# Optimization experiments

Measured on AMD Instinct MI355X. Metric: run time of the kernel, lower is better.

Reference implementation:

```python
import jax, jax.numpy as jnp
import numpy as np

N = 100000          # nodes
MUL = 64            # multiplicity of each irrep in input_1 (64x0e + 64x1o)
O0, O1M, O2M = 320, 128, 64   # output multiplicities: 320x0e + 128x1o + 64x1e
SQRT3 = float(np.sqrt(3.0))
SQRT6 = float(np.sqrt(6.0))
# e3nn path weights: sqrt(dim(ir_out) / sum_paths_to_out(mul1*mul2))
PW0 = float(1.0 / np.sqrt(2.0 * MUL))     # 0e: two paths, x = 128
PW1 = float(np.sqrt(3.0 / (2.0 * MUL)))   # 1o: two paths, x = 128
PW2 = float(np.sqrt(3.0 / MUL))           # 1e: one path,  x = 64


def setup_inputs() -> dict:
    key = jax.random.key(0)
    k = jax.random.split(key, 8)
    return {
        "input_1": jax.random.normal(k[0], (N, 4 * MUL), jnp.float32),  # 64x0e + 64x1o
        "input_2": jax.random.normal(k[1], (N, 4), jnp.float32),        # 1x0e + 1x1o
        "W_a0_o0": jax.random.normal(k[2], (MUL, O0), jnp.float32),     # 0e x 0e -> 0e
        "W_b1_o0": jax.random.normal(k[3], (MUL, O0), jnp.float32),     # 1o x 1o -> 0e
        "W_a1_o1": jax.random.normal(k[4], (MUL, O1M), jnp.float32),    # 0e x 1o -> 1o
        "W_b0_o1": jax.random.normal(k[5], (MUL, O1M), jnp.float32),    # 1o x 0e -> 1o
        "W_b1_o2": jax.random.normal(k[6], (MUL, O2M), jnp.float32),    # 1o x 1o -> 1e
        "bias": jnp.zeros((O0,), jnp.float32),                          # on the 0e scalars
    }


def reference(input_1, input_2, W_a0_o0, W_b1_o0, W_a1_o1, W_b0_o1, W_b1_o2, bias):
    n = input_1.shape[0]
    s_a = input_1[:, :MUL]                        # [N, MUL]      0e block
    v_b = input_1[:, MUL:].reshape(n, MUL, 3)     # [N, MUL, 3]   1o block
    s0 = input_2[:, :1]                           # [N, 1]        0e attr
    v1 = input_2[:, 1:]                           # [N, 3]        1o attr

    # --- 0e output: (0e*0e) and (1o.1o)/sqrt3 (CG delta_ij/sqrt3), fully-connected weights
    dot_b1 = jnp.einsum('nuk,nk->nu', v_b, v1)    # [N, MUL]
    o0 = PW0 * ((s_a * s0) @ W_a0_o0 + (dot_b1 / SQRT3) @ W_b1_o0) + bias  # [N, O0]

    # --- 1o output: (0e x 1o) and (1o x 0e), CG delta/sqrt3
    o1 = (PW1 / SQRT3) * (
        jnp.einsum('nu,uw->nw', s_a, W_a1_o1)[:, :, None] * v1[:, None, :]
        + jnp.einsum('nuk,uw->nwk', v_b, W_b0_o1) * s0[:, :, None]
    )                                             # [N, O1M, 3]

    # --- 1e output: (1o x 1o), CG eps_ijk/sqrt6 -> cross product
    cr = jnp.cross(v_b, v1[:, None, :])           # [N, MUL, 3]
    o2 = (PW2 / SQRT6) * jnp.einsum('nuk,uw->nwk', cr, W_b1_o2)  # [N, O2M, 3]

    return jnp.concatenate([o0, o1.reshape(n, -1), o2.reshape(n, -1)], axis=-1)  # [N, 896]
```

## Files before the change

### kernel.cpp

```cpp
#include <hip/hip_runtime.h>


typedef __bf16 v8bf __attribute__((ext_vector_type(8)));
typedef __bf16 v4bf __attribute__((ext_vector_type(4)));
typedef float f32x4 __attribute__((ext_vector_type(4)));

#define PW0f   0.08838834764831845f
#define PW0S3f 0.05103103630798288f


__global__ __launch_bounds__(256) void prep_weights(
    const float* __restrict__ Wa0, const float* __restrict__ Wb1o0,
    const float* __restrict__ Wa1, const float* __restrict__ Wb0,
    const float* __restrict__ Wo2, unsigned short* __restrict__ ws) {
  int t = blockIdx.x * 256 + threadIdx.x;
  float v; int k, n, base;
  if (t < 20480) {
    k = t / 320; n = t % 320; base = 0;     v = Wa0[k * 320 + n] * PW0f;
  } else if (t < 40960) {
    int tt = t - 20480; k = tt / 320; n = tt % 320; base = 20480; v = Wb1o0[k * 320 + n] * PW0S3f;
  } else if (t < 49152) {
    int tt = t - 40960; k = tt / 128; n = tt % 128; base = 40960; v = Wa1[k * 128 + n] * PW0f;
  } else if (t < 57344) {
    int tt = t - 49152; k = tt / 128; n = tt % 128; base = 49152; v = Wb0[k * 128 + n] * PW0f;
  } else {
    int tt = t - 57344; k = tt / 64;  n = tt % 64;  base = 57344; v = Wo2[k * 64 + n] * PW0f;
  }
  int nt = n >> 4, cc = n & 15, ks = k >> 5, qq = (k >> 3) & 3, j = k & 7;
  int addr = base + ((nt * 2 + ks) * 64 + qq * 16 + cc) * 8 + j;
  __bf16 h = (__bf16)v;
  ws[addr] = __builtin_bit_cast(unsigned short, h);
}

__global__ __launch_bounds__(256, 4) void tp_main(
    const float* __restrict__ in1, const float* __restrict__ in2,
    const float* __restrict__ bias, const unsigned short* __restrict__ wsb,
    float* __restrict__ out, int N) {
  __shared__ __attribute__((aligned(16))) float s0v1[16 * 4];
  __shared__ __attribute__((aligned(16))) __bf16 fsa[1024];
  __shared__ __attribute__((aligned(16))) __bf16 fvb[3][1024];

  const int tid = threadIdx.x;
  const int r0 = blockIdx.x * 16;

  {
    const int m = tid & 15;
    const int g = tid >> 4;
    int rr = r0 + m; if (rr >= N) rr = N - 1;
    const float* rp = in1 + (size_t)rr * 256;
    const float4 sa4 = *(const float4*)(rp + 4 * g);
    const float4 w0  = *(const float4*)(rp + 64 + 12 * g);
    const float4 w1  = *(const float4*)(rp + 64 + 12 * g + 4);
    const float4 w2  = *(const float4*)(rp + 64 + 12 * g + 8);
    const float vf[12] = {w0.x, w0.y, w0.z, w0.w, w1.x, w1.y, w1.z, w1.w,
                          w2.x, w2.y, w2.z, w2.w};
    const int wbase = (((g >> 3) * 64 + ((g >> 1) & 3) * 16 + m) * 8) + 4 * (g & 1);
    v4bf pk;
    pk[0] = (__bf16)sa4.x; pk[1] = (__bf16)sa4.y; pk[2] = (__bf16)sa4.z; pk[3] = (__bf16)sa4.w;
    *(v4bf*)(fsa + wbase) = pk;
#pragma unroll
    for (int c3 = 0; c3 < 3; ++c3) {
      pk[0] = (__bf16)vf[c3]; pk[1] = (__bf16)vf[3 + c3];
      pk[2] = (__bf16)vf[6 + c3]; pk[3] = (__bf16)vf[9 + c3];
      *(v4bf*)(fvb[c3] + wbase) = pk;
    }
    if (tid < 16) {
      int rr2 = r0 + tid; if (rr2 >= N) rr2 = N - 1;
      *(float4*)(s0v1 + tid * 4) = *(const float4*)(in2 + (size_t)rr2 * 4);
    }
  }
  __syncthreads();

  const int lane = tid & 63;
  const int wv = tid >> 6;
  const int c = lane & 15, q = lane >> 4;

  v8bf a_sa[2], a_vb[3][2];
#pragma unroll
  for (int ks = 0; ks < 2; ++ks) {
    a_sa[ks] = *(const v8bf*)(fsa + (ks * 64 + lane) * 8);
#pragma unroll
    for (int c3 = 0; c3 < 3; ++c3)
      a_vb[c3][ks] = *(const v8bf*)(fvb[c3] + (ks * 64 + lane) * 8);
  }
  float4 sv[4];
#pragma unroll
  for (int r = 0; r < 4; ++r) sv[r] = *(const float4*)(s0v1 + (q * 4 + r) * 4);

  const unsigned short* Wa0p = wsb;
  const unsigned short* Wb1p = wsb + 20480;
  const unsigned short* Wa1p = wsb + 40960;
  const unsigned short* Wb0p = wsb + 49152;
  const unsigned short* Wo2p = wsb + 57344;

  for (int job = wv; job < 32; job += 4) {
    if (job < 20) {
      const int nt = job;
      v8bf wa0 = *(const v8bf*)(Wa0p + ((nt * 2 + 0) * 64 + lane) * 8);
      v8bf wa1 = *(const v8bf*)(Wa0p + ((nt * 2 + 1) * 64 + lane) * 8);
      v8bf wb0 = *(const v8bf*)(Wb1p + ((nt * 2 + 0) * 64 + lane) * 8);
      v8bf wb1 = *(const v8bf*)(Wb1p + ((nt * 2 + 1) * 64 + lane) * 8);
      f32x4 ta = {0.f, 0.f, 0.f, 0.f};
      f32x4 tb[3]; tb[0] = ta; tb[1] = ta; tb[2] = ta;
      ta = __builtin_amdgcn_mfma_f32_16x16x32_bf16(a_sa[0], wa0, ta, 0, 0, 0);
      ta = __builtin_amdgcn_mfma_f32_16x16x32_bf16(a_sa[1], wa1, ta, 0, 0, 0);
#pragma unroll
      for (int c3 = 0; c3 < 3; ++c3) {
        tb[c3] = __builtin_amdgcn_mfma_f32_16x16x32_bf16(a_vb[c3][0], wb0, tb[c3], 0, 0, 0);
        tb[c3] = __builtin_amdgcn_mfma_f32_16x16x32_bf16(a_vb[c3][1], wb1, tb[c3], 0, 0, 0);
      }
      const int col = nt * 16 + c;
      const float bv = bias[col];
#pragma unroll
      for (int r = 0; r < 4; ++r) {
        const int gr = r0 + q * 4 + r;
        if (gr < N)
          out[(size_t)gr * 896 + col] =
              bv + sv[r].x * ta[r] + sv[r].y * tb[0][r] + sv[r].z * tb[1][r] + sv[r].w * tb[2][r];
      }
    } else if (job < 28) {
      const int jt = job - 20;
      v8bf ba0 = *(const v8bf*)(Wa1p + ((jt * 2 + 0) * 64 + lane) * 8);
      v8bf ba1 = *(const v8bf*)(Wa1p + ((jt * 2 + 1) * 64 + lane) * 8);
      v8bf bb0 = *(const v8bf*)(Wb0p + ((jt * 2 + 0) * 64 + lane) * 8);
      v8bf bb1 = *(const v8bf*)(Wb0p + ((jt * 2 + 1) * 64 + lane) * 8);
      f32x4 t1 = {0.f, 0.f, 0.f, 0.f};
      f32x4 t2[3]; t2[0] = t1; t2[1] = t1; t2[2] = t1;
      t1 = __builtin_amdgcn_mfma_f32_16x16x32_bf16(a_sa[0], ba0, t1, 0, 0, 0);
      t1 = __builtin_amdgcn_mfma_f32_16x16x32_bf16(a_sa[1], ba1, t1, 0, 0, 0);
#pragma unroll
      for (int c3 = 0; c3 < 3; ++c3) {
        t2[c3] = __builtin_amdgcn_mfma_f32_16x16x32_bf16(a_vb[c3][0], bb0, t2[c3], 0, 0, 0);
        t2[c3] = __builtin_amdgcn_mfma_f32_16x16x32_bf16(a_vb[c3][1], bb1, t2[c3], 0, 0, 0);
      }
#pragma unroll
      for (int r = 0; r < 4; ++r) {
        const int gr = r0 + q * 4 + r;
        if (gr < N) {
          const size_t base = (size_t)gr * 896 + 320 + 3 * (jt * 16 + c);
          out[base + 0] = t1[r] * sv[r].y + t2[0][r] * sv[r].x;
          out[base + 1] = t1[r] * sv[r].z + t2[1][r] * sv[r].x;
          out[base + 2] = t1[r] * sv[r].w + t2[2][r] * sv[r].x;
        }
      }
    } else {
      const int jt = job - 28;
      v8bf b0v = *(const v8bf*)(Wo2p + ((jt * 2 + 0) * 64 + lane) * 8);
      v8bf b1v = *(const v8bf*)(Wo2p + ((jt * 2 + 1) * 64 + lane) * 8);
      f32x4 t3[3];
      t3[0] = f32x4{0.f, 0.f, 0.f, 0.f}; t3[1] = t3[0]; t3[2] = t3[0];
#pragma unroll
      for (int c3 = 0; c3 < 3; ++c3) {
        t3[c3] = __builtin_amdgcn_mfma_f32_16x16x32_bf16(a_vb[c3][0], b0v, t3[c3], 0, 0, 0);
        t3[c3] = __builtin_amdgcn_mfma_f32_16x16x32_bf16(a_vb[c3][1], b1v, t3[c3], 0, 0, 0);
      }
#pragma unroll
      for (int r = 0; r < 4; ++r) {
        const int gr = r0 + q * 4 + r;
        if (gr < N) {
          const size_t base = (size_t)gr * 896 + 704 + 3 * (jt * 16 + c);
          out[base + 0] = t3[1][r] * sv[r].w - t3[2][r] * sv[r].z;
          out[base + 1] = t3[2][r] * sv[r].y - t3[0][r] * sv[r].w;
          out[base + 2] = t3[0][r] * sv[r].z - t3[1][r] * sv[r].y;
        }
      }
    }
  }
}

extern "C" void kernel_launch(void* const* d_in, const int* in_sizes, int n_in,
                              void* d_out, int out_size, void* d_ws, size_t ws_size,
                              hipStream_t stream) {
  const float* in1   = (const float*)d_in[0];
  const float* in2   = (const float*)d_in[1];
  const float* Wa0   = (const float*)d_in[2];
  const float* Wb1o0 = (const float*)d_in[3];
  const float* Wa1   = (const float*)d_in[4];
  const float* Wb0   = (const float*)d_in[5];
  const float* Wo2   = (const float*)d_in[6];
  const float* bias  = (const float*)d_in[7];
  float* out = (float*)d_out;
  unsigned short* ws = (unsigned short*)d_ws;

  const int N = in_sizes[0] / 256;

  hipLaunchKernelGGL(prep_weights, dim3(240), dim3(256), 0, stream,
                     Wa0, Wb1o0, Wa1, Wb0, Wo2, ws);
  const int nblocks = (N + 15) / 16;
  hipLaunchKernelGGL(tp_main, dim3(nblocks), dim3(256), 0, stream,
                     in1, in2, bias, ws, out, N);
}
```

Before: 454.4 us.

## Process 32 rows per 512-thread block with static per-wave job split

Each block now covers 32 rows with 8 waves instead of 16 rows with 4 waves. Each wave owns a fixed set of four output tiles and reuses each weight fragment across two 16-row tiles, which halves weight traffic per row. The first weight fragments are prefetched before the input staging, and bias is staged in shared memory. Full blocks run an unguarded template instantiation, with a separate guarded launch for the remainder. Occupancy can drop with 512-thread blocks, and A fragments are reloaded from LDS per tile instead of being held in registers.

Result: slower. 499.8 us (+10.0%).

```diff
diff --git a/kernel.cpp b/kernel.cpp
--- a/kernel.cpp
+++ b/kernel.cpp
@@ -32,20 +32,49 @@
   ws[addr] = __builtin_bit_cast(unsigned short, h);
 }
 
-__global__ __launch_bounds__(256, 4) void tp_main(
+template <bool GUARD>
+__global__ __launch_bounds__(512, 4) void tp_main(
     const float* __restrict__ in1, const float* __restrict__ in2,
     const float* __restrict__ bias, const unsigned short* __restrict__ wsb,
-    float* __restrict__ out, int N) {
-  __shared__ __attribute__((aligned(16))) float s0v1[16 * 4];
-  __shared__ __attribute__((aligned(16))) __bf16 fsa[1024];
-  __shared__ __attribute__((aligned(16))) __bf16 fvb[3][1024];
+    float* __restrict__ out, int N, int r0base) {
+  __shared__ __attribute__((aligned(16))) float s0v1[32 * 4];
+  __shared__ __attribute__((aligned(16))) float biasl[320];
+  __shared__ __attribute__((aligned(16))) __bf16 fsa[2][1024];
+  __shared__ __attribute__((aligned(16))) __bf16 fvb[2][3][1024];
 
   const int tid = threadIdx.x;
-  const int r0 = blockIdx.x * 16;
+  const int r0 = r0base + blockIdx.x * 32;
+  const int lane = tid & 63;
+  const int wv = tid >> 6;
+
+  const unsigned short* Wa0p = wsb;
+  const unsigned short* Wb1p = wsb + 20480;
+  const unsigned short* Wa1p = wsb + 40960;
+  const unsigned short* Wb0p = wsb + 49152;
+  const unsigned short* Wo2p = wsb + 57344;
+
+  v8bf pf0, pf1, pf2, pf3;
+  if (wv < 5) {
+    const int nt = wv * 4;
+    pf0 = *(const v8bf*)(Wa0p + ((nt * 2 + 0) * 64 + lane) * 8);
+    pf1 = *(const v8bf*)(Wa0p + ((nt * 2 + 1) * 64 + lane) * 8);
+    pf2 = *(const v8bf*)(Wb1p + ((nt * 2 + 0) * 64 + lane) * 8);
+    pf3 = *(const v8bf*)(Wb1p + ((nt * 2 + 1) * 64 + lane) * 8);
+  } else if (wv < 7) {
+    const int jt = (wv - 5) * 4;
+    pf0 = *(const v8bf*)(Wa1p + ((jt * 2 + 0) * 64 + lane) * 8);
+    pf1 = *(const v8bf*)(Wa1p + ((jt * 2 + 1) * 64 + lane) * 8);
+    pf2 = *(const v8bf*)(Wb0p + ((jt * 2 + 0) * 64 + lane) * 8);
+    pf3 = *(const v8bf*)(Wb0p + ((jt * 2 + 1) * 64 + lane) * 8);
+  } else {
+    pf0 = *(const v8bf*)(Wo2p + ((0 * 64 + lane)) * 8);
+    pf1 = *(const v8bf*)(Wo2p + ((1 * 64 + lane)) * 8);
+    pf2 = pf0; pf3 = pf1;
+  }
 
   {
-    const int m = tid & 15;
-    const int g = tid >> 4;
+    const int m = tid & 31;
+    const int g = tid >> 5;
     int rr = r0 + m; if (rr >= N) rr = N - 1;
     const float* rp = in1 + (size_t)rr * 256;
     const float4 sa4 = *(const float4*)(rp + 4 * g);
@@ -54,114 +83,132 @@
     const float4 w2  = *(const float4*)(rp + 64 + 12 * g + 8);
     const float vf[12] = {w0.x, w0.y, w0.z, w0.w, w1.x, w1.y, w1.z, w1.w,
                           w2.x, w2.y, w2.z, w2.w};
-    const int wbase = (((g >> 3) * 64 + ((g >> 1) & 3) * 16 + m) * 8) + 4 * (g & 1);
+    const int ts = m >> 4, mm = m & 15;
+    const int wbase = (((g >> 3) * 64 + ((g >> 1) & 3) * 16 + mm) * 8) + 4 * (g & 1);
     v4bf pk;
     pk[0] = (__bf16)sa4.x; pk[1] = (__bf16)sa4.y; pk[2] = (__bf16)sa4.z; pk[3] = (__bf16)sa4.w;
-    *(v4bf*)(fsa + wbase) = pk;
+    *(v4bf*)(&fsa[ts][wbase]) = pk;
 #pragma unroll
     for (int c3 = 0; c3 < 3; ++c3) {
       pk[0] = (__bf16)vf[c3]; pk[1] = (__bf16)vf[3 + c3];
       pk[2] = (__bf16)vf[6 + c3]; pk[3] = (__bf16)vf[9 + c3];
-      *(v4bf*)(fvb[c3] + wbase) = pk;
-    }
-    if (tid < 16) {
+      *(v4bf*)(&fvb[ts][c3][wbase]) = pk;
+    }
+    if (tid < 32) {
       int rr2 = r0 + tid; if (rr2 >= N) rr2 = N - 1;
       *(float4*)(s0v1 + tid * 4) = *(const float4*)(in2 + (size_t)rr2 * 4);
     }
+    if (tid < 80) *(float4*)(biasl + tid * 4) = *(const float4*)(bias + tid * 4);
   }
   __syncthreads();
 
-  const int lane = tid & 63;
-  const int wv = tid >> 6;
   const int c = lane & 15, q = lane >> 4;
 
-  v8bf a_sa[2], a_vb[3][2];
-#pragma unroll
-  for (int ks = 0; ks < 2; ++ks) {
-    a_sa[ks] = *(const v8bf*)(fsa + (ks * 64 + lane) * 8);
-#pragma unroll
-    for (int c3 = 0; c3 < 3; ++c3)
-      a_vb[c3][ks] = *(const v8bf*)(fvb[c3] + (ks * 64 + lane) * 8);
-  }
-  float4 sv[4];
-#pragma unroll
-  for (int r = 0; r < 4; ++r) sv[r] = *(const float4*)(s0v1 + (q * 4 + r) * 4);
-
-  const unsigned short* Wa0p = wsb;
-  const unsigned short* Wb1p = wsb + 20480;
-  const unsigned short* Wa1p = wsb + 40960;
-  const unsigned short* Wb0p = wsb + 49152;
-  const unsigned short* Wo2p = wsb + 57344;
-
-  for (int job = wv; job < 32; job += 4) {
-    if (job < 20) {
-      const int nt = job;
-      v8bf wa0 = *(const v8bf*)(Wa0p + ((nt * 2 + 0) * 64 + lane) * 8);
-      v8bf wa1 = *(const v8bf*)(Wa0p + ((nt * 2 + 1) * 64 + lane) * 8);
-      v8bf wb0 = *(const v8bf*)(Wb1p + ((nt * 2 + 0) * 64 + lane) * 8);
-      v8bf wb1 = *(const v8bf*)(Wb1p + ((nt * 2 + 1) * 64 + lane) * 8);
-      f32x4 ta = {0.f, 0.f, 0.f, 0.f};
-      f32x4 tb[3]; tb[0] = ta; tb[1] = ta; tb[2] = ta;
-      ta = __builtin_amdgcn_mfma_f32_16x16x32_bf16(a_sa[0], wa0, ta, 0, 0, 0);
-      ta = __builtin_amdgcn_mfma_f32_16x16x32_bf16(a_sa[1], wa1, ta, 0, 0, 0);
-#pragma unroll
-      for (int c3 = 0; c3 < 3; ++c3) {
-        tb[c3] = __builtin_amdgcn_mfma_f32_16x16x32_bf16(a_vb[c3][0], wb0, tb[c3], 0, 0, 0);
-        tb[c3] = __builtin_amdgcn_mfma_f32_16x16x32_bf16(a_vb[c3][1], wb1, tb[c3], 0, 0, 0);
+  if (wv < 5) {
+#pragma unroll
+    for (int j = 0; j < 4; ++j) {
+      const int nt = wv * 4 + j;
+      const v8bf wa0 = j ? *(const v8bf*)(Wa0p + ((nt * 2 + 0) * 64 + lane) * 8) : pf0;
+      const v8bf wa1 = j ? *(const v8bf*)(Wa0p + ((nt * 2 + 1) * 64 + lane) * 8) : pf1;
+      const v8bf wb0 = j ? *(const v8bf*)(Wb1p + ((nt * 2 + 0) * 64 + lane) * 8) : pf2;
+      const v8bf wb1 = j ? *(const v8bf*)(Wb1p + ((nt * 2 + 1) * 64 + lane) * 8) : pf3;
+      const int col = nt * 16 + c;
+      const float bv = biasl[col];
+#pragma unroll
+      for (int t = 0; t < 2; ++t) {
+        f32x4 ta = {0.f, 0.f, 0.f, 0.f};
+        f32x4 tb[3]; tb[0] = ta; tb[1] = ta; tb[2] = ta;
+        {
+          const v8bf a0 = *(const v8bf*)(&fsa[t][(lane) * 8]);
+          const v8bf a1 = *(const v8bf*)(&fsa[t][(64 + lane) * 8]);
+          ta = __builtin_amdgcn_mfma_f32_16x16x32_bf16(a0, wa0, ta, 0, 0, 0);
+          ta = __builtin_amdgcn_mfma_f32_16x16x32_bf16(a1, wa1, ta, 0, 0, 0);
+        }
+#pragma unroll
+        for (int c3 = 0; c3 < 3; ++c3) {
+          const v8bf b0 = *(const v8bf*)(&fvb[t][c3][(lane) * 8]);
+          const v8bf b1 = *(const v8bf*)(&fvb[t][c3][(64 + lane) * 8]);
+          tb[c3] = __builtin_amdgcn_mfma_f32_16x16x32_bf16(b0, wb0, tb[c3], 0, 0, 0);
+          tb[c3] = __builtin_amdgcn_mfma_f32_16x16x32_bf16(b1, wb1, tb[c3], 0, 0, 0);
+        }
+#pragma unroll
+        for (int r = 0; r < 4; ++r) {
+          const int row = t * 16 + q * 4 + r;
+          const int gr = r0 + row;
+          const float4 s = *(const float4*)(s0v1 + row * 4);
+          if (!GUARD || gr < N)
+            out[(size_t)gr * 896 + col] =
+                bv + s.x * ta[r] + s.y * tb[0][r] + s.z * tb[1][r] + s.w * tb[2][r];
+        }
       }
-      const int col = nt * 16 + c;
-      const float bv = bias[col];
-#pragma unroll
-      for (int r = 0; r < 4; ++r) {
-        const int gr = r0 + q * 4 + r;
-        if (gr < N)
-          out[(size_t)gr * 896 + col] =
-              bv + sv[r].x * ta[r] + sv[r].y * tb[0][r] + sv[r].z * tb[1][r] + sv[r].w * tb[2][r];
+    }
+  } else if (wv < 7) {
+#pragma unroll
+    for (int j = 0; j < 4; ++j) {
+      const int jt = (wv - 5) * 4 + j;
+      const v8bf ba0 = j ? *(const v8bf*)(Wa1p + ((jt * 2 + 0) * 64 + lane) * 8) : pf0;
+      const v8bf ba1 = j ? *(const v8bf*)(Wa1p + ((jt * 2 + 1) * 64 + lane) * 8) : pf1;
+      const v8bf bb0 = j ? *(const v8bf*)(Wb0p + ((jt * 2 + 0) * 64 + lane) * 8) : pf2;
+      const v8bf bb1 = j ? *(const v8bf*)(Wb0p + ((jt * 2 + 1) * 64 + lane) * 8) : pf3;
+#pragma unroll
+      for (int t = 0; t < 2; ++t) {
+        f32x4 t1 = {0.f, 0.f, 0.f, 0.f};
+        f32x4 t2[3]; t2[0] = t1; t2[1] = t1; t2[2] = t1;
+        {
+          const v8bf a0 = *(const v8bf*)(&fsa[t][(lane) * 8]);
+          const v8bf a1 = *(const v8bf*)(&fsa[t][(64 + lane) * 8]);
+          t1 = __builtin_amdgcn_mfma_f32_16x16x32_bf16(a0, ba0, t1, 0, 0, 0);
+          t1 = __builtin_amdgcn_mfma_f32_16x16x32_bf16(a1, ba1, t1, 0, 0, 0);
+        }
+#pragma unroll
+        for (int c3 = 0; c3 < 3; ++c3) {
+          const v8bf b0 = *(const v8bf*)(&fvb[t][c3][(lane) * 8]);
+          const v8bf b1 = *(const v8bf*)(&fvb[t][c3][(64 + lane) * 8]);
+          t2[c3] = __builtin_amdgcn_mfma_f32_16x16x32_bf16(b0, bb0, t2[c3], 0, 0, 0);
+          t2[c3] = __builtin_amdgcn_mfma_f32_16x16x32_bf16(b1, bb1, t2[c3], 0, 0, 0);
+        }
+#pragma unroll
+        for (int r = 0; r < 4; ++r) {
+          const int row = t * 16 + q * 4 + r;
+          const int gr = r0 + row;
+          const float4 s = *(const float4*)(s0v1 + row * 4);
+          if (!GUARD || gr < N) {
+            const size_t base = (size_t)gr * 896 + 320 + 3 * (jt * 16 + c);
+            out[base + 0] = t1[r] * s.y + t2[0][r] * s.x;
+            out[base + 1] = t1[r] * s.z + t2[1][r] * s.x;
+            out[base + 2] = t1[r] * s.w + t2[2][r] * s.x;
+          }
+        }
       }
-    } else if (job < 28) {
-      const int jt = job - 20;
-      v8bf ba0 = *(const v8bf*)(Wa1p + ((jt * 2 + 0) * 64 + lane) * 8);
-      v8bf ba1 = *(const v8bf*)(Wa1p + ((jt * 2 + 1) * 64 + lane) * 8);
-      v8bf bb0 = *(const v8bf*)(Wb0p + ((jt * 2 + 0) * 64 + lane) * 8);
-      v8bf bb1 = *(const v8bf*)(Wb0p + ((jt * 2 + 1) * 64 + lane) * 8);
-      f32x4 t1 = {0.f, 0.f, 0.f, 0.f};
-      f32x4 t2[3]; t2[0] = t1; t2[1] = t1; t2[2] = t1;
-      t1 = __builtin_amdgcn_mfma_f32_16x16x32_bf16(a_sa[0], ba0, t1, 0, 0, 0);
-      t1 = __builtin_amdgcn_mfma_f32_16x16x32_bf16(a_sa[1], ba1, t1, 0, 0, 0);
-#pragma unroll
-      for (int c3 = 0; c3 < 3; ++c3) {
-        t2[c3] = __builtin_amdgcn_mfma_f32_16x16x32_bf16(a_vb[c3][0], bb0, t2[c3], 0, 0, 0);
-        t2[c3] = __builtin_amdgcn_mfma_f32_16x16x32_bf16(a_vb[c3][1], bb1, t2[c3], 0, 0, 0);
-      }
-#pragma unroll
-      for (int r = 0; r < 4; ++r) {
-        const int gr = r0 + q * 4 + r;
-        if (gr < N) {
-          const size_t base = (size_t)gr * 896 + 320 + 3 * (jt * 16 + c);
-          out[base + 0] = t1[r] * sv[r].y + t2[0][r] * sv[r].x;
-          out[base + 1] = t1[r] * sv[r].z + t2[1][r] * sv[r].x;
-          out[base + 2] = t1[r] * sv[r].w + t2[2][r] * sv[r].x;
-        }
-      }
-    } else {
-      const int jt = job - 28;
-      v8bf b0v = *(const v8bf*)(Wo2p + ((jt * 2 + 0) * 64 + lane) * 8);
-      v8bf b1v = *(const v8bf*)(Wo2p + ((jt * 2 + 1) * 64 + lane) * 8);
-      f32x4 t3[3];
-      t3[0] = f32x4{0.f, 0.f, 0.f, 0.f}; t3[1] = t3[0]; t3[2] = t3[0];
-#pragma unroll
-      for (int c3 = 0; c3 < 3; ++c3) {
-        t3[c3] = __builtin_amdgcn_mfma_f32_16x16x32_bf16(a_vb[c3][0], b0v, t3[c3], 0, 0, 0);
-        t3[c3] = __builtin_amdgcn_mfma_f32_16x16x32_bf16(a_vb[c3][1], b1v, t3[c3], 0, 0, 0);
-      }
-#pragma unroll
-      for (int r = 0; r < 4; ++r) {
-        const int gr = r0 + q * 4 + r;
-        if (gr < N) {
-          const size_t base = (size_t)gr * 896 + 704 + 3 * (jt * 16 + c);
-          out[base + 0] = t3[1][r] * sv[r].w - t3[2][r] * sv[r].z;
-          out[base + 1] = t3[2][r] * sv[r].y - t3[0][r] * sv[r].w;
-          out[base + 2] = t3[0][r] * sv[r].z - t3[1][r] * sv[r].y;
+    }
+  } else {
+#pragma unroll
+    for (int j = 0; j < 4; ++j) {
+      const int jt = j;
+      const v8bf b0v = j ? *(const v8bf*)(Wo2p + ((jt * 2 + 0) * 64 + lane) * 8) : pf0;
+      const v8bf b1v = j ? *(const v8bf*)(Wo2p + ((jt * 2 + 1) * 64 + lane) * 8) : pf1;
+#pragma unroll
+      for (int t = 0; t < 2; ++t) {
+        f32x4 t3[3];
+        t3[0] = f32x4{0.f, 0.f, 0.f, 0.f}; t3[1] = t3[0]; t3[2] = t3[0];
+#pragma unroll
+        for (int c3 = 0; c3 < 3; ++c3) {
+          const v8bf a0 = *(const v8bf*)(&fvb[t][c3][(lane) * 8]);
+          const v8bf a1 = *(const v8bf*)(&fvb[t][c3][(64 + lane) * 8]);
+          t3[c3] = __builtin_amdgcn_mfma_f32_16x16x32_bf16(a0, b0v, t3[c3], 0, 0, 0);
+          t3[c3] = __builtin_amdgcn_mfma_f32_16x16x32_bf16(a1, b1v, t3[c3], 0, 0, 0);
+        }
+#pragma unroll
+        for (int r = 0; r < 4; ++r) {
+          const int row = t * 16 + q * 4 + r;
+          const int gr = r0 + row;
+          const float4 s = *(const float4*)(s0v1 + row * 4);
+          if (!GUARD || gr < N) {
+            const size_t base = (size_t)gr * 896 + 704 + 3 * (jt * 16 + c);
+            out[base + 0] = t3[1][r] * s.w - t3[2][r] * s.z;
+            out[base + 1] = t3[2][r] * s.y - t3[0][r] * s.w;
+            out[base + 2] = t3[0][r] * s.z - t3[1][r] * s.y;
+          }
         }
       }
     }
@@ -186,7 +233,11 @@
 
   hipLaunchKernelGGL(prep_weights, dim3(240), dim3(256), 0, stream,
                      Wa0, Wb1o0, Wa1, Wb0, Wo2, ws);
-  const int nblocks = (N + 15) / 16;
-  hipLaunchKernelGGL(tp_main, dim3(nblocks), dim3(256), 0, stream,
-                     in1, in2, bias, ws, out, N);
+
+  const int nfull = N >> 5;
+  if (nfull > 0)
+    tp_main<false><<<dim3(nfull), dim3(512), 0, stream>>>(in1, in2, bias, ws, out, N, 0);
+  const int rem = N & 31;
+  if (rem)
+    tp_main<true><<<dim3(1), dim3(512), 0, stream>>>(in1, in2, bias, ws, out, N, nfull * 32);
 }
```
